# Kernel optimization log

Hardware: AMD Instinct MI355X
Metric: run time of the kernel (lower is better)

Reference implementation:

```python
import jax, jax.numpy as jnp
import numpy as np

M, K1, N1, N2, N3 = 131072, 256, 1024, 1024, 256


def setup_inputs() -> dict:
    key = jax.random.key(0)
    k_x, k1, k2, k3 = jax.random.split(key, 4)
    x = jax.random.normal(k_x, (M, K1), dtype=jnp.float32)
    # Kaiming-ish scaling so softplus stays in a sane range
    w1 = jax.random.normal(k1, (K1, N1), dtype=jnp.float32) * (1.0 / np.sqrt(K1))
    w2 = jax.random.normal(k2, (N1, N2), dtype=jnp.float32) * (1.0 / np.sqrt(N1))
    w3 = jax.random.normal(k3, (N2, N3), dtype=jnp.float32) * (1.0 / np.sqrt(N2))
    return {"x": x, "w1": w1, "w2": w2, "w3": w3}


def reference(x, w1, w2, w3):
    # Fused 3-layer MLP: out = softplus(softplus(x @ W1) @ W2) @ W3
    h1 = jax.nn.softplus(x @ w1)   # [M, N1]
    h2 = jax.nn.softplus(h1 @ w2)  # [M, N2]
    return h2 @ w3                 # [M, N3]
```

## Files before the change

### kernel.cpp

```cpp
#include <hip/hip_runtime.h>

typedef __attribute__((ext_vector_type(8))) short short8;
typedef __attribute__((ext_vector_type(4))) float floatx4;
typedef __attribute__((ext_vector_type(2))) unsigned int uintx2;
typedef __attribute__((ext_vector_type(4))) unsigned int uintx4;
typedef unsigned short u16;

#define MFMA(a, b, c) __builtin_amdgcn_mfma_f32_16x16x32_bf16((a), (b), (c), 0, 0, 0)

__device__ __forceinline__ u16 f2bf(float f) {
  unsigned int u = __builtin_bit_cast(unsigned int, f);
  u += ((u >> 16) & 1u) + 0x7fffu;
  return (u16)(u >> 16);
}

__device__ __forceinline__ float softplus_f(float v) {
  float a = __builtin_fabsf(v);
  float e = __expf(-a);
  float l = __logf(1.0f + e);
  return __builtin_fmaxf(v, 0.0f) + l;
}

__device__ __forceinline__ unsigned int pack_sp(float lo, float hi) {
  return (unsigned int)f2bf(softplus_f(lo)) | ((unsigned int)f2bf(softplus_f(hi)) << 16);
}

__global__ void transpose_cvt(const float* __restrict__ in, u16* __restrict__ out, int K, int N) {
  __shared__ float tile[32][33];
  const int bn = blockIdx.x * 32, bk = blockIdx.y * 32;
  const int tx = threadIdx.x, ty = threadIdx.y;
#pragma unroll
  for (int i = 0; i < 32; i += 8)
    tile[ty + i][tx] = in[(size_t)(bk + ty + i) * N + bn + tx];
  __syncthreads();
#pragma unroll
  for (int i = 0; i < 32; i += 8)
    out[(size_t)(bn + ty + i) * K + bk + tx] = f2bf(tile[tx][ty + i]);
}

__device__ __forceinline__ void gld16(const void* g, void* l) {
  __builtin_amdgcn_global_load_lds((const __attribute__((address_space(1))) void*)g,
                                   (__attribute__((address_space(3))) void*)l, 16, 0, 0);
}

template <int LN>
__device__ __forceinline__ void vwait() {
  if constexpr (LN == 0) asm volatile("s_waitcnt vmcnt(0)" ::: "memory");
  else if constexpr (LN == 2) asm volatile("s_waitcnt vmcnt(2)" ::: "memory");
  else if constexpr (LN == 3) asm volatile("s_waitcnt vmcnt(3)" ::: "memory");
  else if constexpr (LN == 4) asm volatile("s_waitcnt vmcnt(4)" ::: "memory");
}

template <int K, int EPI, int BM, bool ACTF32>
__global__ __launch_bounds__(512, 2) void gemmk2(const void* __restrict__ actv,
                                                 const u16* __restrict__ wt,
                                                 void* __restrict__ Cout, int N, int nbn) {
  constexpr int JA = BM / 128;
  constexpr int MT = BM / 32;
  constexpr int HALF_A = BM * 32;
  constexpr int HALF_T = HALF_A + 8192;
  constexpr int H = K / 32;
  constexpr int LV = JA + 2;
  __shared__ u16 lds[4 * HALF_T];
  u16* L = lds;
  const int tid = threadIdx.x, lane = tid & 63, wv = tid >> 6;
  const int l15 = lane & 15, g = lane >> 4;
  const int wvm = wv >> 2, wvn = wv & 3;
  const int nwg = gridDim.x, o = blockIdx.x;
  const int sw = (o & 7) * (nwg >> 3) + (o >> 3);
  const int bm = sw / nbn, bn = sw % nbn;
  const size_t am0 = (size_t)bm * BM;
  const size_t wn0 = (size_t)bn * 256;

  int bfo[MT], afo[4];
#pragma unroll
  for (int mt = 0; mt < MT; ++mt) {
    const int r = wvm * (BM / 2) + mt * 16 + l15;
    bfo[mt] = (r * 4 + (g ^ ((r >> 1) & 3))) * 8;
  }
#pragma unroll
  for (int t = 0; t < 4; ++t) {
    const int r = wvn * 64 + t * 16 + l15;
    afo[t] = HALF_A + (r * 4 + (g ^ ((r >> 1) & 3))) * 8;
  }
  const int rt = tid >> 2, ggt = (tid & 3) ^ ((rt >> 1) & 3);
  const int dstt = tid * 8;
  const u16* asrcb = nullptr;
  const float* fsrcb = nullptr;
  if constexpr (ACTF32) fsrcb = (const float*)actv + (am0 + rt) * K + ggt * 8;
  else asrcb = (const u16*)actv + (am0 + rt) * K + ggt * 8;
  const u16* wsrcb = wt + (wn0 + rt) * K + ggt * 8;

#define STG_W(hh)                                                                  \
  _Pragma("unroll") for (int j = 0; j < 2; ++j)                                    \
      gld16(wsrcb + (size_t)j * 128 * K + (hh) * 32,                               \
            L + ((hh) & 3) * HALF_T + HALF_A + j * 4096 + dstt);
#define STG_A(hh)                                                                  \
  _Pragma("unroll") for (int j = 0; j < JA; ++j)                                   \
      gld16(asrcb + (size_t)j * 128 * K + (hh) * 32,                               \
            L + ((hh) & 3) * HALF_T + j * 4096 + dstt);
#define STG_F_LOAD(hh, AV)                                                         \
  _Pragma("unroll") for (int j = 0; j < JA; ++j) {                                 \
    AV[j][0] = *(const floatx4*)(fsrcb + (size_t)j * 128 * K + (hh) * 32);         \
    AV[j][1] = *(const floatx4*)(fsrcb + (size_t)j * 128 * K + (hh) * 32 + 4);     \
  }
#define STG_F_WRITE(hh, AV)                                                        \
  _Pragma("unroll") for (int j = 0; j < JA; ++j) {                                 \
    uintx4 w_;                                                                     \
    w_.x = (unsigned)f2bf(AV[j][0].x) | ((unsigned)f2bf(AV[j][0].y) << 16);        \
    w_.y = (unsigned)f2bf(AV[j][0].z) | ((unsigned)f2bf(AV[j][0].w) << 16);        \
    w_.z = (unsigned)f2bf(AV[j][1].x) | ((unsigned)f2bf(AV[j][1].y) << 16);        \
    w_.w = (unsigned)f2bf(AV[j][1].z) | ((unsigned)f2bf(AV[j][1].w) << 16);        \
    *(uintx4*)(L + ((hh) & 3) * HALF_T + j * 4096 + dstt) = w_;                    \
  }

  floatx4 acc[4][MT];
  const floatx4 z4 = {0.f, 0.f, 0.f, 0.f};
#pragma unroll
  for (int t = 0; t < 4; ++t)
#pragma unroll
    for (int mt = 0; mt < MT; ++mt) acc[t][mt] = z4;

  short8 bfA[MT], bfB[MT], afA[4], afB[4];

  if constexpr (ACTF32) {
    floatx4 av[JA][2];
    STG_F_LOAD(0, av) STG_W(0)
    vwait<2>();
    STG_F_WRITE(0, av)
    STG_F_LOAD(1, av) STG_W(1)
    vwait<2>();
    STG_F_WRITE(1, av)
    asm volatile("s_waitcnt lgkmcnt(0)" ::: "memory");
  } else {
    STG_A(0) STG_W(0)
    STG_A(1) STG_W(1)
    vwait<LV>();
  }
  __builtin_amdgcn_s_barrier();
  asm volatile("" ::: "memory");
#pragma unroll
  for (int mt = 0; mt < MT; ++mt) bfA[mt] = *(const short8*)(L + bfo[mt]);
#pragma unroll
  for (int t = 0; t < 4; ++t) afA[t] = *(const short8*)(L + afo[t]);

#define PHASE_BODY(p_, CAF, CBF, NAF, NBF)                                         \
  {                                                                                \
    if ((p_) + 2 < H) {                                                            \
      if constexpr (ACTF32) {                                                      \
        floatx4 av[JA][2];                                                         \
        STG_F_LOAD((p_) + 2, av)                                                   \
        STG_W((p_) + 2)                                                            \
        vwait<2>();                                                                \
        STG_F_WRITE((p_) + 2, av)                                                  \
      } else {                                                                     \
        STG_A((p_) + 2)                                                            \
        STG_W((p_) + 2)                                                            \
        vwait<LV>();                                                               \
      }                                                                            \
    } else {                                                                       \
      vwait<0>();                                                                  \
    }                                                                              \
    __builtin_amdgcn_s_barrier();                                                  \
    asm volatile("" ::: "memory");                                                 \
    if ((p_) + 1 < H) {                                                            \
      const int sn_ = (((p_) + 1) & 3) * HALF_T;                                   \
      _Pragma("unroll") for (int mt = 0; mt < MT; ++mt)                            \
          NBF[mt] = *(const short8*)(L + sn_ + bfo[mt]);                           \
      _Pragma("unroll") for (int t = 0; t < 4; ++t)                                \
          NAF[t] = *(const short8*)(L + sn_ + afo[t]);                             \
    }                                                                              \
    __builtin_amdgcn_s_setprio(1);                                                 \
    _Pragma("unroll") for (int t = 0; t < 4; ++t)                                  \
        _Pragma("unroll") for (int mt = 0; mt < MT; ++mt)                          \
            acc[t][mt] = MFMA(CAF[t], CBF[mt], acc[t][mt]);                        \
    __builtin_amdgcn_s_setprio(0);                                                 \
    if constexpr (ACTF32) asm volatile("s_waitcnt lgkmcnt(0)" ::: "memory");       \
    asm volatile("" ::: "memory");                                                 \
    __builtin_amdgcn_s_barrier();                                                  \
    asm volatile("" ::: "memory");                                                 \
  }

#pragma unroll 1
  for (int it = 0; it < H / 2; ++it) {
    PHASE_BODY(2 * it, afA, bfA, afB, bfB)
    PHASE_BODY(2 * it + 1, afB, bfB, afA, bfA)
  }
#undef PHASE_BODY
#undef STG_W
#undef STG_A
#undef STG_F_LOAD
#undef STG_F_WRITE

  if constexpr (EPI == 0) {
    u16* cl = L;
#pragma unroll
    for (int t = 0; t < 4; ++t)
#pragma unroll
      for (int mt = 0; mt < MT; ++mt) {
        const int m = wvm * (BM / 2) + mt * 16 + l15;
        const int n0 = wvn * 64 + t * 16 + g * 4;
        const int j = n0 >> 3, hh = (n0 >> 2) & 1;
        uintx2 pk;
        pk.x = pack_sp(acc[t][mt].x, acc[t][mt].y);
        pk.y = pack_sp(acc[t][mt].z, acc[t][mt].w);
        *(uintx2*)(cl + m * 256 + ((j ^ (m & 7)) << 3) + (hh << 2)) = pk;
      }
    __syncthreads();
    u16* outp = (u16*)Cout;
#pragma unroll
    for (int i = 0; i < BM / 16; ++i) {
      const int c = i * 512 + tid;
      const int m = c >> 5, j = c & 31;
      uintx4 v = *(const uintx4*)(cl + m * 256 + ((j ^ (m & 7)) << 3));
      *(uintx4*)(outp + (am0 + m) * N + wn0 + j * 8) = v;
    }
  } else {
    float* cf = (float*)L;
    constexpr int R = BM / 2;
#pragma unroll
    for (int q = 0; q < 2; ++q) {
      if (q) __syncthreads();
      if (wvm == q) {
#pragma unroll
        for (int t = 0; t < 4; ++t)
#pragma unroll
          for (int mt = 0; mt < MT; ++mt) {
            const int m = mt * 16 + l15;
            const int p = (wvn * 64 + t * 16 + g * 4) >> 1;
            *(floatx4*)(cf + m * 256 + ((p ^ ((m & 7) << 1)) << 1)) = acc[t][mt];
          }
      }
      __syncthreads();
      float* outp = (float*)Cout;
#pragma unroll
      for (int i = 0; i < R / 8; ++i) {
        const int c = i * 512 + tid;
        const int m = c >> 6, cc = c & 63;
        const int p = cc * 2;
        floatx4 v = *(const floatx4*)(cf + m * 256 + ((p ^ ((m & 7) << 1)) << 1));
        *(floatx4*)(outp + (am0 + q * R + m) * N + wn0 + cc * 4) = v;
      }
    }
  }
}

__global__ __launch_bounds__(512, 2) void mlp3_fused(const float* __restrict__ x,
                                                     const u16* __restrict__ w1t,
                                                     const u16* __restrict__ w2t,
                                                     const u16* __restrict__ w3t,
                                                     float* __restrict__ out) {
  __shared__ u16 h1s[64 * 1024];
  __shared__ u16 xs[64 * 256];
  const int tid = threadIdx.x, lane = tid & 63, wv = tid >> 6;
  const int l15 = lane & 15, g = lane >> 4;
  const size_t m0 = (size_t)blockIdx.x * 64;
  const floatx4 z4 = {0.f, 0.f, 0.f, 0.f};
  {
    const float* xp = x + m0 * 256;
#pragma unroll
    for (int r = 0; r < 8; ++r) {
      int idx4 = r * 512 + tid;
      int m = idx4 >> 6, k = (idx4 & 63) << 2;
      floatx4 v = *(const floatx4*)(xp + m * 256 + k);
      uintx2 pk;
      pk.x = (unsigned)f2bf(v.x) | ((unsigned)f2bf(v.y) << 16);
      pk.y = (unsigned)f2bf(v.z) | ((unsigned)f2bf(v.w) << 16);
      *(uintx2*)(xs + ((m * 256 + k) ^ ((m & 7) << 3))) = pk;
    }
  }
  __syncthreads();
#pragma unroll 1
  for (int c = 0; c < 4; ++c) {
    floatx4 acc[2][4];
#pragma unroll
    for (int t = 0; t < 2; ++t)
#pragma unroll
      for (int mt = 0; mt < 4; ++mt) acc[t][mt] = z4;
    const u16* p0 = w1t + (size_t)(c * 256 + wv * 32 + l15) * 256;
#pragma unroll
    for (int ks = 0; ks < 8; ++ks) {
      const int k = ks * 32 + g * 8;
      short8 a0 = *(const short8*)(p0 + k);
      short8 a1 = *(const short8*)(p0 + 16 * 256 + k);
      short8 b0 = *(const short8*)(xs + (((0 * 16 + l15) * 256 + k) ^ ((l15 & 7) << 3)));
      short8 b1 = *(const short8*)(xs + (((1 * 16 + l15) * 256 + k) ^ ((l15 & 7) << 3)));
      short8 b2 = *(const short8*)(xs + (((2 * 16 + l15) * 256 + k) ^ ((l15 & 7) << 3)));
      short8 b3 = *(const short8*)(xs + (((3 * 16 + l15) * 256 + k) ^ ((l15 & 7) << 3)));
      acc[0][0] = MFMA(a0, b0, acc[0][0]); acc[0][1] = MFMA(a0, b1, acc[0][1]);
      acc[0][2] = MFMA(a0, b2, acc[0][2]); acc[0][3] = MFMA(a0, b3, acc[0][3]);
      acc[1][0] = MFMA(a1, b0, acc[1][0]); acc[1][1] = MFMA(a1, b1, acc[1][1]);
      acc[1][2] = MFMA(a1, b2, acc[1][2]); acc[1][3] = MFMA(a1, b3, acc[1][3]);
    }
#pragma unroll
    for (int t = 0; t < 2; ++t)
#pragma unroll
      for (int mt = 0; mt < 4; ++mt) {
        const int n1 = c * 256 + wv * 32 + t * 16 + g * 4;
        const int m = mt * 16 + l15;
        uintx2 pk;
        pk.x = pack_sp(acc[t][mt].x, acc[t][mt].y);
        pk.y = pack_sp(acc[t][mt].z, acc[t][mt].w);
        *(uintx2*)(h1s + ((m * 1024 + n1) ^ ((m & 7) << 3))) = pk;
      }
  }
  __syncthreads();
  floatx4 acc3[2][4];
#pragma unroll
  for (int t = 0; t < 2; ++t)
#pragma unroll
    for (int mt = 0; mt < 4; ++mt) acc3[t][mt] = z4;
#pragma unroll 1
  for (int c2 = 0; c2 < 4; ++c2) {
    floatx4 acc2[2][4];
#pragma unroll
    for (int t = 0; t < 2; ++t)
#pragma unroll
      for (int mt = 0; mt < 4; ++mt) acc2[t][mt] = z4;
    {
      const u16* p0 = w2t + (size_t)(c2 * 256 + wv * 32 + l15) * 1024;
#pragma unroll 4
      for (int ks = 0; ks < 32; ++ks) {
        const int k = ks * 32 + g * 8;
        short8 a0 = *(const short8*)(p0 + k);
        short8 a1 = *(const short8*)(p0 + 16 * 1024 + k);
        short8 b0 = *(const short8*)(h1s + (((0 * 16 + l15) * 1024 + k) ^ ((l15 & 7) << 3)));
        short8 b1 = *(const short8*)(h1s + (((1 * 16 + l15) * 1024 + k) ^ ((l15 & 7) << 3)));
        short8 b2 = *(const short8*)(h1s + (((2 * 16 + l15) * 1024 + k) ^ ((l15 & 7) << 3)));
        short8 b3 = *(const short8*)(h1s + (((3 * 16 + l15) * 1024 + k) ^ ((l15 & 7) << 3)));
        acc2[0][0] = MFMA(a0, b0, acc2[0][0]); acc2[0][1] = MFMA(a0, b1, acc2[0][1]);
        acc2[0][2] = MFMA(a0, b2, acc2[0][2]); acc2[0][3] = MFMA(a0, b3, acc2[0][3]);
        acc2[1][0] = MFMA(a1, b0, acc2[1][0]); acc2[1][1] = MFMA(a1, b1, acc2[1][1]);
        acc2[1][2] = MFMA(a1, b2, acc2[1][2]); acc2[1][3] = MFMA(a1, b3, acc2[1][3]);
      }
    }
    __syncthreads();
#pragma unroll
    for (int t = 0; t < 2; ++t)
#pragma unroll
      for (int mt = 0; mt < 4; ++mt) {
        const int n2l = wv * 32 + t * 16 + g * 4;
        const int m = mt * 16 + l15;
        uintx2 pk;
        pk.x = pack_sp(acc2[t][mt].x, acc2[t][mt].y);
        pk.y = pack_sp(acc2[t][mt].z, acc2[t][mt].w);
        *(uintx2*)(xs + ((m * 256 + n2l) ^ ((m & 7) << 3))) = pk;
      }
    __syncthreads();
    {
      const u16* p0 = w3t + (size_t)(wv * 32 + l15) * 1024 + c2 * 256;
#pragma unroll
      for (int ks = 0; ks < 8; ++ks) {
        const int k = ks * 32 + g * 8;
        short8 a0 = *(const short8*)(p0 + k);
        short8 a1 = *(const short8*)(p0 + 16 * 1024 + k);
        short8 b0 = *(const short8*)(xs + (((0 * 16 + l15) * 256 + k) ^ ((l15 & 7) << 3)));
        short8 b1 = *(const short8*)(xs + (((1 * 16 + l15) * 256 + k) ^ ((l15 & 7) << 3)));
        short8 b2 = *(const short8*)(xs + (((2 * 16 + l15) * 256 + k) ^ ((l15 & 7) << 3)));
        short8 b3 = *(const short8*)(xs + (((3 * 16 + l15) * 256 + k) ^ ((l15 & 7) << 3)));
        acc3[0][0] = MFMA(a0, b0, acc3[0][0]); acc3[0][1] = MFMA(a0, b1, acc3[0][1]);
        acc3[0][2] = MFMA(a0, b2, acc3[0][2]); acc3[0][3] = MFMA(a0, b3, acc3[0][3]);
        acc3[1][0] = MFMA(a1, b0, acc3[1][0]); acc3[1][1] = MFMA(a1, b1, acc3[1][1]);
        acc3[1][2] = MFMA(a1, b2, acc3[1][2]); acc3[1][3] = MFMA(a1, b3, acc3[1][3]);
      }
    }
  }
#pragma unroll
  for (int t = 0; t < 2; ++t)
#pragma unroll
    for (int mt = 0; mt < 4; ++mt) {
      const int n3 = wv * 32 + t * 16 + g * 4;
      const int m = mt * 16 + l15;
      *(floatx4*)(out + (m0 + m) * 256 + n3) = acc3[t][mt];
    }
}

extern "C" void kernel_launch(void* const* d_in, const int* in_sizes, int n_in,
                              void* d_out, int out_size, void* d_ws, size_t ws_size,
                              hipStream_t stream) {
  const float* x = (const float*)d_in[0];
  const float* w1 = (const float*)d_in[1];
  const float* w2 = (const float*)d_in[2];
  const float* w3 = (const float*)d_in[3];
  float* out = (float*)d_out;
  const size_t M = 131072;

  u16* w1t = (u16*)d_ws;
  u16* w2t = w1t + 1024 * 256;
  u16* w3t = w2t + 1024 * 1024;
  u16* bufA = w3t + 256 * 1024;
  const size_t weights_el = 1024 * 256 + 1024 * 1024 + 256 * 1024;

  size_t CM = 0;
  const size_t cands[4] = {32768, 16384, 8192, 4096};
  for (int i = 0; i < 4; ++i) {
    size_t need = (weights_el + 2 * cands[i] * 1024) * sizeof(u16);
    if (ws_size >= need) { CM = cands[i]; break; }
  }

  dim3 tb(32, 8);
  transpose_cvt<<<dim3(32, 8), tb, 0, stream>>>(w1, w1t, 256, 1024);
  transpose_cvt<<<dim3(32, 32), tb, 0, stream>>>(w2, w2t, 1024, 1024);
  transpose_cvt<<<dim3(8, 32), tb, 0, stream>>>(w3, w3t, 1024, 256);

  if (CM) {
    u16* bufB = bufA + CM * 1024;
    const int nchunk = (int)(M / CM);
    for (int ci = 0; ci < nchunk; ++ci) {
      const float* xc = x + (size_t)ci * CM * 256;
      float* oc = out + (size_t)ci * CM * 256;
      gemmk2<256, 0, 256, true><<<(int)(CM / 256) * 4, 512, 0, stream>>>(xc, w1t, bufA, 1024, 4);
      gemmk2<1024, 0, 256, false><<<(int)(CM / 256) * 4, 512, 0, stream>>>(bufA, w2t, bufB, 1024, 4);
      gemmk2<1024, 1, 128, false><<<(int)(CM / 128), 512, 0, stream>>>(bufB, w3t, oc, 256, 1);
    }
  } else {
    mlp3_fused<<<M / 64, 512, 0, stream>>>(x, w1t, w2t, w3t, out);
  }
}
```

Baseline: 718.1 us.

## Load weight fragments directly into registers and drop weight LDS staging

The GEMM kernel now reads each wave's weight MFMA fragments straight from global memory into registers, prefetching one K-step ahead. Only the activation tile is staged in shared memory, using a 4-slot ring with a single barrier per phase instead of two. This cuts weight LDS writes and reads and one barrier per phase. In exchange, weights are re-read from global or cache by each wave row, and global-load latency has to be hidden with only one phase of register prefetch.

```diff
diff --git a/kernel.cpp b/kernel.cpp
--- a/kernel.cpp
+++ b/kernel.cpp
@@ -46,22 +46,22 @@
 template <int LN>
 __device__ __forceinline__ void vwait() {
   if constexpr (LN == 0) asm volatile("s_waitcnt vmcnt(0)" ::: "memory");
-  else if constexpr (LN == 2) asm volatile("s_waitcnt vmcnt(2)" ::: "memory");
-  else if constexpr (LN == 3) asm volatile("s_waitcnt vmcnt(3)" ::: "memory");
   else if constexpr (LN == 4) asm volatile("s_waitcnt vmcnt(4)" ::: "memory");
+  else if constexpr (LN == 9) asm volatile("s_waitcnt vmcnt(9)" ::: "memory");
+  else if constexpr (LN == 10) asm volatile("s_waitcnt vmcnt(10)" ::: "memory");
+  else if constexpr (LN == 12) asm volatile("s_waitcnt vmcnt(12)" ::: "memory");
 }
 
 template <int K, int EPI, int BM, bool ACTF32>
-__global__ __launch_bounds__(512, 2) void gemmk2(const void* __restrict__ actv,
-                                                 const u16* __restrict__ wt,
-                                                 void* __restrict__ Cout, int N, int nbn) {
+__global__ __launch_bounds__(512, 2) void gemmw(const void* __restrict__ actv,
+                                                const u16* __restrict__ wt,
+                                                void* __restrict__ Cout, int N, int nbn) {
   constexpr int JA = BM / 128;
   constexpr int MT = BM / 32;
-  constexpr int HALF_A = BM * 32;
-  constexpr int HALF_T = HALF_A + 8192;
+  constexpr int SLOT = BM * 32;
   constexpr int H = K / 32;
-  constexpr int LV = JA + 2;
-  __shared__ u16 lds[4 * HALF_T];
+  constexpr int LSZ = BM * 256;
+  __shared__ u16 lds[LSZ];
   u16* L = lds;
   const int tid = threadIdx.x, lane = tid & 63, wv = tid >> 6;
   const int l15 = lane & 15, g = lane >> 4;
@@ -72,47 +72,22 @@
   const size_t am0 = (size_t)bm * BM;
   const size_t wn0 = (size_t)bn * 256;
 
-  int bfo[MT], afo[4];
+  int bfo[MT];
 #pragma unroll
   for (int mt = 0; mt < MT; ++mt) {
     const int r = wvm * (BM / 2) + mt * 16 + l15;
     bfo[mt] = (r * 4 + (g ^ ((r >> 1) & 3))) * 8;
   }
-#pragma unroll
-  for (int t = 0; t < 4; ++t) {
-    const int r = wvn * 64 + t * 16 + l15;
-    afo[t] = HALF_A + (r * 4 + (g ^ ((r >> 1) & 3))) * 8;
-  }
+  const u16* wp[4];
+#pragma unroll
+  for (int t = 0; t < 4; ++t)
+    wp[t] = wt + (wn0 + wvn * 64 + t * 16 + l15) * (size_t)K + g * 8;
   const int rt = tid >> 2, ggt = (tid & 3) ^ ((rt >> 1) & 3);
   const int dstt = tid * 8;
-  const u16* asrcb = nullptr;
-  const float* fsrcb = nullptr;
-  if constexpr (ACTF32) fsrcb = (const float*)actv + (am0 + rt) * K + ggt * 8;
-  else asrcb = (const u16*)actv + (am0 + rt) * K + ggt * 8;
-  const u16* wsrcb = wt + (wn0 + rt) * K + ggt * 8;
-
-#define STG_W(hh)                                                                  \
-  _Pragma("unroll") for (int j = 0; j < 2; ++j)                                    \
-      gld16(wsrcb + (size_t)j * 128 * K + (hh) * 32,                               \
-            L + ((hh) & 3) * HALF_T + HALF_A + j * 4096 + dstt);
-#define STG_A(hh)                                                                  \
-  _Pragma("unroll") for (int j = 0; j < JA; ++j)                                   \
-      gld16(asrcb + (size_t)j * 128 * K + (hh) * 32,                               \
-            L + ((hh) & 3) * HALF_T + j * 4096 + dstt);
-#define STG_F_LOAD(hh, AV)                                                         \
-  _Pragma("unroll") for (int j = 0; j < JA; ++j) {                                 \
-    AV[j][0] = *(const floatx4*)(fsrcb + (size_t)j * 128 * K + (hh) * 32);         \
-    AV[j][1] = *(const floatx4*)(fsrcb + (size_t)j * 128 * K + (hh) * 32 + 4);     \
-  }
-#define STG_F_WRITE(hh, AV)                                                        \
-  _Pragma("unroll") for (int j = 0; j < JA; ++j) {                                 \
-    uintx4 w_;                                                                     \
-    w_.x = (unsigned)f2bf(AV[j][0].x) | ((unsigned)f2bf(AV[j][0].y) << 16);        \
-    w_.y = (unsigned)f2bf(AV[j][0].z) | ((unsigned)f2bf(AV[j][0].w) << 16);        \
-    w_.z = (unsigned)f2bf(AV[j][1].x) | ((unsigned)f2bf(AV[j][1].y) << 16);        \
-    w_.w = (unsigned)f2bf(AV[j][1].z) | ((unsigned)f2bf(AV[j][1].w) << 16);        \
-    *(uintx4*)(L + ((hh) & 3) * HALF_T + j * 4096 + dstt) = w_;                    \
-  }
+  const u16* asrc = nullptr;
+  const float* fsrc = nullptr;
+  if constexpr (ACTF32) fsrc = (const float*)actv + (am0 + rt) * K + ggt * 8;
+  else asrc = (const u16*)actv + (am0 + rt) * K + ggt * 8;
 
   floatx4 acc[4][MT];
   const floatx4 z4 = {0.f, 0.f, 0.f, 0.f};
@@ -121,76 +96,79 @@
 #pragma unroll
     for (int mt = 0; mt < MT; ++mt) acc[t][mt] = z4;
 
-  short8 bfA[MT], bfB[MT], afA[4], afB[4];
+  short8 wfA[4], wfB[4];
+
+#define STG_BF16(hh)                                                              \
+  _Pragma("unroll") for (int j = 0; j < JA; ++j)                                  \
+      gld16(asrc + (size_t)j * 128 * K + (hh) * 32,                               \
+            L + ((hh) & 3) * SLOT + j * 4096 + dstt);
+#define STG_F32(hh)                                                               \
+  {                                                                               \
+    floatx4 av[JA][2];                                                            \
+    _Pragma("unroll") for (int j = 0; j < JA; ++j) {                              \
+      av[j][0] = *(const floatx4*)(fsrc + (size_t)j * 128 * K + (hh) * 32);       \
+      av[j][1] = *(const floatx4*)(fsrc + (size_t)j * 128 * K + (hh) * 32 + 4);   \
+    }                                                                             \
+    _Pragma("unroll") for (int j = 0; j < JA; ++j) {                              \
+      uintx4 w_;                                                                  \
+      w_.x = (unsigned)f2bf(av[j][0].x) | ((unsigned)f2bf(av[j][0].y) << 16);     \
+      w_.y = (unsigned)f2bf(av[j][0].z) | ((unsigned)f2bf(av[j][0].w) << 16);     \
+      w_.z = (unsigned)f2bf(av[j][1].x) | ((unsigned)f2bf(av[j][1].y) << 16);     \
+      w_.w = (unsigned)f2bf(av[j][1].z) | ((unsigned)f2bf(av[j][1].w) << 16);     \
+      *(uintx4*)(L + ((hh) & 3) * SLOT + j * 4096 + dstt) = w_;                   \
+    }                                                                             \
+  }
 
   if constexpr (ACTF32) {
-    floatx4 av[JA][2];
-    STG_F_LOAD(0, av) STG_W(0)
-    vwait<2>();
-    STG_F_WRITE(0, av)
-    STG_F_LOAD(1, av) STG_W(1)
-    vwait<2>();
-    STG_F_WRITE(1, av)
-    asm volatile("s_waitcnt lgkmcnt(0)" ::: "memory");
+    STG_F32(0)
+    STG_F32(1)
   } else {
-    STG_A(0) STG_W(0)
-    STG_A(1) STG_W(1)
-    vwait<LV>();
-  }
-  __builtin_amdgcn_s_barrier();
-  asm volatile("" ::: "memory");
-#pragma unroll
-  for (int mt = 0; mt < MT; ++mt) bfA[mt] = *(const short8*)(L + bfo[mt]);
-#pragma unroll
-  for (int t = 0; t < 4; ++t) afA[t] = *(const short8*)(L + afo[t]);
-
-#define PHASE_BODY(p_, CAF, CBF, NAF, NBF)                                         \
-  {                                                                                \
-    if ((p_) + 2 < H) {                                                            \
-      if constexpr (ACTF32) {                                                      \
-        floatx4 av[JA][2];                                                         \
-        STG_F_LOAD((p_) + 2, av)                                                   \
-        STG_W((p_) + 2)                                                            \
-        vwait<2>();                                                                \
-        STG_F_WRITE((p_) + 2, av)                                                  \
-      } else {                                                                     \
-        STG_A((p_) + 2)                                                            \
-        STG_W((p_) + 2)                                                            \
-        vwait<LV>();                                                               \
-      }                                                                            \
-    } else {                                                                       \
-      vwait<0>();                                                                  \
-    }                                                                              \
-    __builtin_amdgcn_s_barrier();                                                  \
-    asm volatile("" ::: "memory");                                                 \
-    if ((p_) + 1 < H) {                                                            \
-      const int sn_ = (((p_) + 1) & 3) * HALF_T;                                   \
-      _Pragma("unroll") for (int mt = 0; mt < MT; ++mt)                            \
-          NBF[mt] = *(const short8*)(L + sn_ + bfo[mt]);                           \
-      _Pragma("unroll") for (int t = 0; t < 4; ++t)                                \
-          NAF[t] = *(const short8*)(L + sn_ + afo[t]);                             \
-    }                                                                              \
-    __builtin_amdgcn_s_setprio(1);                                                 \
-    _Pragma("unroll") for (int t = 0; t < 4; ++t)                                  \
-        _Pragma("unroll") for (int mt = 0; mt < MT; ++mt)                          \
-            acc[t][mt] = MFMA(CAF[t], CBF[mt], acc[t][mt]);                        \
-    __builtin_amdgcn_s_setprio(0);                                                 \
-    if constexpr (ACTF32) asm volatile("s_waitcnt lgkmcnt(0)" ::: "memory");       \
-    asm volatile("" ::: "memory");                                                 \
-    __builtin_amdgcn_s_barrier();                                                  \
-    asm volatile("" ::: "memory");                                                 \
+    STG_BF16(0)
+    STG_BF16(1)
+  }
+#pragma unroll
+  for (int t = 0; t < 4; ++t) wfA[t] = *(const short8*)(wp[t]);
+
+#define PHASE(p_, WC, WN)                                                         \
+  {                                                                               \
+    if ((p_) + 1 < H) {                                                           \
+      _Pragma("unroll") for (int t = 0; t < 4; ++t)                               \
+          WN[t] = *(const short8*)(wp[t] + ((p_) + 1) * 32);                      \
+    }                                                                             \
+    if constexpr (ACTF32) {                                                       \
+      if ((p_) + 2 < H) STG_F32((p_) + 2)                                         \
+      asm volatile("s_waitcnt lgkmcnt(0)" ::: "memory");                          \
+    } else {                                                                      \
+      if ((p_) + 2 < H) STG_BF16((p_) + 2)                                        \
+      if ((p_) < H - 2) vwait<8 + 2 * JA>();                                      \
+      else if ((p_) == H - 2) vwait<8 + JA>();                                    \
+      else vwait<4>();                                                            \
+    }                                                                             \
+    __builtin_amdgcn_s_barrier();                                                 \
+    asm volatile("" ::: "memory");                                                \
+    short8 bf[MT];                                                                \
+    const int sl_ = ((p_) & 3) * SLOT;                                            \
+    _Pragma("unroll") for (int mt = 0; mt < MT; ++mt)                             \
+        bf[mt] = *(const short8*)(L + sl_ + bfo[mt]);                             \
+    __builtin_amdgcn_s_setprio(1);                                                \
+    _Pragma("unroll") for (int mt = 0; mt < MT; ++mt)                             \
+        _Pragma("unroll") for (int t = 0; t < 4; ++t)                             \
+            acc[t][mt] = MFMA(WC[t], bf[mt], acc[t][mt]);                         \
+    __builtin_amdgcn_s_setprio(0);                                                \
+    asm volatile("" ::: "memory");                                                \
   }
 
 #pragma unroll 1
   for (int it = 0; it < H / 2; ++it) {
-    PHASE_BODY(2 * it, afA, bfA, afB, bfB)
-    PHASE_BODY(2 * it + 1, afB, bfB, afA, bfA)
-  }
-#undef PHASE_BODY
-#undef STG_W
-#undef STG_A
-#undef STG_F_LOAD
-#undef STG_F_WRITE
+    const int p0 = 2 * it, p1 = 2 * it + 1;
+    PHASE(p0, wfA, wfB)
+    PHASE(p1, wfB, wfA)
+  }
+#undef PHASE
+#undef STG_BF16
+#undef STG_F32
+
+  __syncthreads();
 
   if constexpr (EPI == 0) {
     u16* cl = L;
@@ -409,9 +387,9 @@
     for (int ci = 0; ci < nchunk; ++ci) {
       const float* xc = x + (size_t)ci * CM * 256;
       float* oc = out + (size_t)ci * CM * 256;
-      gemmk2<256, 0, 256, true><<<(int)(CM / 256) * 4, 512, 0, stream>>>(xc, w1t, bufA, 1024, 4);
-      gemmk2<1024, 0, 256, false><<<(int)(CM / 256) * 4, 512, 0, stream>>>(bufA, w2t, bufB, 1024, 4);
-      gemmk2<1024, 1, 128, false><<<(int)(CM / 128), 512, 0, stream>>>(bufB, w3t, oc, 256, 1);
+      gemmw<256, 0, 256, true><<<(int)(CM / 256) * 4, 512, 0, stream>>>(xc, w1t, bufA, 1024, 4);
+      gemmw<1024, 0, 256, false><<<(int)(CM / 256) * 4, 512, 0, stream>>>(bufA, w2t, bufB, 1024, 4);
+      gemmw<1024, 1, 128, false><<<(int)(CM / 128), 512, 0, stream>>>(bufB, w3t, oc, 256, 1);
     }
   } else {
     mlp3_fused<<<M / 64, 512, 0, stream>>>(x, w1t, w2t, w3t, out);
```

After: 796.2 us. 10.9% more time.
